# Performance work log

Hardware: AMD Instinct MI355X
Metric: run time of the kernel (lower is better)

The kernel has to match this reference:

```python
import jax, jax.numpy as jnp
import numpy as np

BIDAT = 4


def _biatt(atoms_vector, amino_vector, U, Wp2c, bp2c, Wc2p, bc2p,
           Whc, bhc, Whp, bhp, Wac, bac, Wap, bap, Wcc, bcc, Wcp, bcp):
    cfs, pfs = [], []
    for i in range(BIDAT):  # fixed small structural loop (4 distinct param sets)
        # bilinear tanh affinity: [Na, Np]
        A = jnp.tanh((atoms_vector @ U[i]) @ amino_vector.T)
        atoms_trans = A @ jnp.tanh(amino_vector @ Wp2c[i] + bp2c[i])      # [Na, D]
        amino_trans = A.T @ jnp.tanh(atoms_vector @ Wc2p[i] + bc2p[i])    # [Np, D]
        atoms_tmp = jnp.concatenate(
            [jnp.tanh(atoms_vector @ Whc[i] + bhc[i]), atoms_trans], axis=1)  # [Na, 2D]
        amino_tmp = jnp.concatenate(
            [jnp.tanh(amino_vector @ Whp[i] + bhp[i]), amino_trans], axis=1)  # [Np, 2D]
        # NOTE: softmax over axis=1 of a [N,1] tensor == all-ones (faithful to torch source)
        atoms_att = jax.nn.softmax(atoms_tmp @ Wac[i] + bac[i], axis=1)   # [Na, 1]
        amino_att = jax.nn.softmax(amino_tmp @ Wap[i] + bap[i], axis=1)   # [Np, 1]
        cfs.append(atoms_vector * atoms_att)
        pfs.append(amino_vector * amino_att)
    cf_final = jnp.concatenate(cfs, axis=1) @ Wcc + bcc   # [Na, D]
    pf_final = jnp.concatenate(pfs, axis=1) @ Wcp + bcp   # [Np, D]
    return cf_final, pf_final


def setup_inputs() -> dict:
    D, Na, Np = 512, 6144, 6144
    key = jax.random.key(0)
    ks = jax.random.split(key, 20)
    s = 0.04  # ~xavier-scale init for D=512
    return {
        "atoms_vector": jax.random.normal(ks[0], (Na, D), jnp.float32),
        "amino_vector": jax.random.normal(ks[1], (Np, D), jnp.float32),
        "U":    jax.random.normal(ks[2], (BIDAT, D, D), jnp.float32) * s,
        "Wp2c": jax.random.normal(ks[3], (BIDAT, D, D), jnp.float32) * s,
        "bp2c": jnp.zeros((BIDAT, D), jnp.float32),
        "Wc2p": jax.random.normal(ks[4], (BIDAT, D, D), jnp.float32) * s,
        "bc2p": jnp.zeros((BIDAT, D), jnp.float32),
        "Whc":  jax.random.normal(ks[5], (BIDAT, D, D), jnp.float32) * s,
        "bhc":  jnp.zeros((BIDAT, D), jnp.float32),
        "Whp":  jax.random.normal(ks[6], (BIDAT, D, D), jnp.float32) * s,
        "bhp":  jnp.zeros((BIDAT, D), jnp.float32),
        "Wac":  jax.random.normal(ks[7], (BIDAT, 2 * D, 1), jnp.float32) * s,
        "bac":  jnp.zeros((BIDAT, 1), jnp.float32),
        "Wap":  jax.random.normal(ks[8], (BIDAT, 2 * D, 1), jnp.float32) * s,
        "bap":  jnp.zeros((BIDAT, 1), jnp.float32),
        "Wcc":  jax.random.normal(ks[9], (BIDAT * D, D), jnp.float32) * s,
        "bcc":  jnp.zeros((D,), jnp.float32),
        "Wcp":  jax.random.normal(ks[10], (BIDAT * D, D), jnp.float32) * s,
        "bcp":  jnp.zeros((D,), jnp.float32),
    }


def reference(atoms_vector, amino_vector, U, Wp2c, bp2c, Wc2p, bc2p,
              Whc, bhc, Whp, bhp, Wac, bac, Wap, bap, Wcc, bcc, Wcp, bcp):
    return _biatt(atoms_vector, amino_vector, U, Wp2c, bp2c, Wc2p, bc2p,
                  Whc, bhc, Whp, bhp, Wac, bac, Wap, bap, Wcc, bcc, Wcp, bcp)
```

## Files before the change

kernel.cpp:

```cpp
#include <hip/hip_runtime.h>
#include <hip/hip_bf16.h>

#define DDIM 512
#define NROWS 6144
#define BM 64
#define BN 128
#define BK 32
#define KSTEPS (DDIM / BK)

typedef __attribute__((ext_vector_type(8))) short short8;
typedef __attribute__((ext_vector_type(4))) float f32x4;

#define GLDS16(g, s)                                          \
  __builtin_amdgcn_global_load_lds(                           \
      (const __attribute__((address_space(1))) void*)(g),     \
      (__attribute__((address_space(3))) void*)(s), 16, 0, 0)

__global__ __launch_bounds__(256) void prep_w(
    const float* __restrict__ Wcc, const float* __restrict__ Wcp,
    __hip_bfloat16* __restrict__ Wt) {
    const float* W = blockIdx.z ? Wcp : Wcc;
    unsigned short* o = (unsigned short*)Wt + (size_t)blockIdx.z * DDIM * DDIM;
    __shared__ float lds[32][65];
    const int k0 = blockIdx.x * 32, n0 = blockIdx.y * 64;
    #pragma unroll
    for (int u = 0; u < 2; ++u) {
        int idx = u * 256 + threadIdx.x;
        int kk = idx >> 4, c = idx & 15;
        float4 s = {0.f, 0.f, 0.f, 0.f};
        #pragma unroll
        for (int i = 0; i < 4; ++i) {
            float4 v = *(const float4*)&W[(size_t)(i * DDIM + k0 + kk) * DDIM + n0 + c * 4];
            s.x += v.x; s.y += v.y; s.z += v.z; s.w += v.w;
        }
        lds[kk][c * 4 + 0] = s.x;
        lds[kk][c * 4 + 1] = s.y;
        lds[kk][c * 4 + 2] = s.z;
        lds[kk][c * 4 + 3] = s.w;
    }
    __syncthreads();
    #pragma unroll
    for (int u = 0; u < 2; ++u) {
        int idx = u * 256 + threadIdx.x;
        int nr = idx >> 3, kc = idx & 7;
        ushort4 p;
        #pragma unroll
        for (int j = 0; j < 4; ++j) {
            __hip_bfloat16 h = __float2bfloat16(lds[kc * 4 + j][nr]);
            ((unsigned short*)&p)[j] = *(unsigned short*)&h;
        }
        *(ushort4*)&o[(size_t)(n0 + nr) * DDIM + k0 + kc * 4] = p;
    }
}

__global__ __launch_bounds__(256, 3) void gemm_bias(
    const float* __restrict__ Aat, const float* __restrict__ Aam,
    const __hip_bfloat16* __restrict__ Wtall,
    const float* __restrict__ bias0, const float* __restrict__ bias1,
    float* __restrict__ C) {
  __shared__ float As[3][BM * BK];
  __shared__ unsigned short Bs[3][BN * BK];

  const int z = blockIdx.z;
  const float* A = z ? Aam : Aat;
  const unsigned short* Wt = (const unsigned short*)Wtall + (size_t)z * DDIM * DDIM;
  const float* bias = z ? bias1 : bias0;
  float* Cz = C + (size_t)z * NROWS * DDIM;

  const int tid = threadIdx.x;
  const int w = tid >> 6, l = tid & 63;
  const int m0 = blockIdx.x * BM;
  const int n0 = blockIdx.y * BN;

  const float* srcA0;
  const float* srcA1;
  const unsigned short* srcB0;
  const unsigned short* srcB1;
  {
    int r0 = w * 16 + (l >> 3);
    int r1 = r0 + 8;
    srcA0 = A + (size_t)(m0 + r0) * DDIM + (((l & 7) ^ (r0 & 7)) << 2);
    srcA1 = A + (size_t)(m0 + r1) * DDIM + (((l & 7) ^ (r1 & 7)) << 2);
    int q0 = w * 32 + (l >> 2);
    int q1 = q0 + 16;
    srcB0 = Wt + (size_t)(n0 + q0) * DDIM + (((l & 3) ^ ((q0 >> 1) & 3)) << 3);
    srcB1 = Wt + (size_t)(n0 + q1) * DDIM + (((l & 3) ^ ((q1 >> 1) & 3)) << 3);
  }
  const unsigned ldsA0 = (w * 2 + 0) * 256, ldsA1 = (w * 2 + 1) * 256;
  const unsigned ldsB0 = (w * 2 + 0) * 512, ldsB1 = (w * 2 + 1) * 512;

#define STAGE(buf, kk)                                 \
  do {                                                 \
    GLDS16(srcA0 + (kk) * BK, &As[buf][ldsA0]);        \
    GLDS16(srcA1 + (kk) * BK, &As[buf][ldsA1]);        \
    GLDS16(srcB0 + (kk) * BK, &Bs[buf][ldsB0]);        \
    GLDS16(srcB1 + (kk) * BK, &Bs[buf][ldsB1]);        \
  } while (0)

  f32x4 acc[2][4];
  #pragma unroll
  for (int i = 0; i < 2; ++i)
    #pragma unroll
    for (int j = 0; j < 4; ++j) acc[i][j] = (f32x4){0.f, 0.f, 0.f, 0.f};

  const int s0 = (l >> 4) * 2;
  const int bs = (l >> 4);
  const int lr = l & 15;

#define COMPUTE(buf)                                                          \
  do {                                                                        \
    short8 afr[2];                                                            \
    _Pragma("unroll")                                                         \
    for (int tm = 0; tm < 2; ++tm) {                                          \
      int r = (w >> 1) * 32 + tm * 16 + lr;                                   \
      f32x4 x0 = *(const f32x4*)&As[buf][r * BK + (((s0 + 0) ^ (r & 7)) << 2)]; \
      f32x4 x1 = *(const f32x4*)&As[buf][r * BK + (((s0 + 1) ^ (r & 7)) << 2)]; \
      float xv[8] = {x0[0], x0[1], x0[2], x0[3], x1[0], x1[1], x1[2], x1[3]}; \
      _Pragma("unroll")                                                       \
      for (int e = 0; e < 8; ++e) {                                           \
        __hip_bfloat16 h = __float2bfloat16(xv[e]);                           \
        afr[tm][e] = *(short*)&h;                                             \
      }                                                                       \
    }                                                                         \
    _Pragma("unroll")                                                         \
    for (int tn = 0; tn < 4; ++tn) {                                          \
      int r = (w & 1) * 64 + tn * 16 + lr;                                    \
      short8 bf = *(const short8*)&Bs[buf][r * BK + ((bs ^ ((r >> 1) & 3)) << 3)]; \
      acc[0][tn] = __builtin_amdgcn_mfma_f32_16x16x32_bf16(afr[0], bf, acc[0][tn], 0, 0, 0); \
      acc[1][tn] = __builtin_amdgcn_mfma_f32_16x16x32_bf16(afr[1], bf, acc[1][tn], 0, 0, 0); \
    }                                                                         \
  } while (0)

  STAGE(0, 0);
  STAGE(1, 1);

  #pragma unroll
  for (int t = 0; t < KSTEPS; ++t) {
    if (t < KSTEPS - 1)
      asm volatile("s_waitcnt vmcnt(4)" ::: "memory");
    else
      asm volatile("s_waitcnt vmcnt(0)" ::: "memory");
    __builtin_amdgcn_s_barrier();
    if (t + 2 < KSTEPS) STAGE((t + 2) % 3, t + 2);
    COMPUTE(t % 3);
  }

  const int rg = (l >> 4) * 4;
  #pragma unroll
  for (int tn = 0; tn < 4; ++tn) {
    const int col = n0 + (w & 1) * 64 + tn * 16 + lr;
    const float bv = bias[col];
    #pragma unroll
    for (int tm = 0; tm < 2; ++tm) {
      const int row = m0 + (w >> 1) * 32 + tm * 16 + rg;
      #pragma unroll
      for (int r = 0; r < 4; ++r)
        Cz[(size_t)(row + r) * DDIM + col] = acc[tm][tn][r] + bv;
    }
  }
#undef STAGE
#undef COMPUTE
}

extern "C" void kernel_launch(void* const* d_in, const int* in_sizes, int n_in,
                              void* d_out, int out_size, void* d_ws, size_t ws_size,
                              hipStream_t stream) {
    const float* atoms = (const float*)d_in[0];
    const float* amino = (const float*)d_in[1];
    const float* Wcc   = (const float*)d_in[15];
    const float* bcc   = (const float*)d_in[16];
    const float* Wcp   = (const float*)d_in[17];
    const float* bcp   = (const float*)d_in[18];
    float* out = (float*)d_out;

    __hip_bfloat16* Wt = (__hip_bfloat16*)d_ws;

    dim3 fgrid(DDIM / 32, DDIM / 64, 2);
    prep_w<<<fgrid, 256, 0, stream>>>(Wcc, Wcp, Wt);

    dim3 ggrid(NROWS / BM, DDIM / BN, 2);
    gemm_bias<<<ggrid, 256, 0, stream>>>(atoms, amino, Wt, bcc, bcp, out);
}
```

Baseline: 134.1 us.

## Keep full weight panel resident in LDS and drop per-step block barriers

The GEMM tile shrinks to 64x64. The block's entire 64x512 bf16 weight panel is now loaded into LDS once up front, replacing the per-k-step staging of B tiles. Each wave streams and converts only its own 16 activation rows through a private double buffer. That removes the block-wide barrier from the k-loop, leaving only vmcnt/lgkmcnt waits. In exchange, the grid doubles, each activation row is read twice as many times from L2/HBM, per-wave MFMA work per step drops, and LDS use rises to roughly 80KB per block, which limits occupancy to two blocks.

```diff
diff --git a/kernel.cpp b/kernel.cpp
--- a/kernel.cpp
+++ b/kernel.cpp
@@ -4,7 +4,7 @@
 #define DDIM 512
 #define NROWS 6144
 #define BM 64
-#define BN 128
+#define BN 64
 #define BK 32
 #define KSTEPS (DDIM / BK)
 
@@ -53,13 +53,13 @@
     }
 }
 
-__global__ __launch_bounds__(256, 3) void gemm_bias(
+__global__ __launch_bounds__(256, 2) void gemm_bias(
     const float* __restrict__ Aat, const float* __restrict__ Aam,
     const __hip_bfloat16* __restrict__ Wtall,
     const float* __restrict__ bias0, const float* __restrict__ bias1,
     float* __restrict__ C) {
-  __shared__ float As[3][BM * BK];
-  __shared__ unsigned short Bs[3][BN * BK];
+  __shared__ unsigned short Bs[BN * DDIM];
+  __shared__ float As[2][BM * BK];
 
   const int z = blockIdx.z;
   const float* A = z ? Aam : Aat;
@@ -69,97 +69,81 @@
 
   const int tid = threadIdx.x;
   const int w = tid >> 6, l = tid & 63;
-  const int m0 = blockIdx.x * BM;
-  const int n0 = blockIdx.y * BN;
+  const int lr = l & 15, hi = l >> 4;
+  const int m0 = blockIdx.x * BM, n0 = blockIdx.y * BN;
 
-  const float* srcA0;
-  const float* srcA1;
-  const unsigned short* srcB0;
-  const unsigned short* srcB1;
-  {
-    int r0 = w * 16 + (l >> 3);
-    int r1 = r0 + 8;
-    srcA0 = A + (size_t)(m0 + r0) * DDIM + (((l & 7) ^ (r0 & 7)) << 2);
-    srcA1 = A + (size_t)(m0 + r1) * DDIM + (((l & 7) ^ (r1 & 7)) << 2);
-    int q0 = w * 32 + (l >> 2);
-    int q1 = q0 + 16;
-    srcB0 = Wt + (size_t)(n0 + q0) * DDIM + (((l & 3) ^ ((q0 >> 1) & 3)) << 3);
-    srcB1 = Wt + (size_t)(n0 + q1) * DDIM + (((l & 3) ^ ((q1 >> 1) & 3)) << 3);
+  #pragma unroll
+  for (int r = 0; r < 16; ++r) {
+    const int row = w * 16 + r;
+    GLDS16(Wt + (size_t)(n0 + row) * DDIM + ((l ^ (row & 7)) << 3),
+           &Bs[row * DDIM]);
   }
-  const unsigned ldsA0 = (w * 2 + 0) * 256, ldsA1 = (w * 2 + 1) * 256;
-  const unsigned ldsB0 = (w * 2 + 0) * 512, ldsB1 = (w * 2 + 1) * 512;
 
-#define STAGE(buf, kk)                                 \
-  do {                                                 \
-    GLDS16(srcA0 + (kk) * BK, &As[buf][ldsA0]);        \
-    GLDS16(srcA1 + (kk) * BK, &As[buf][ldsA1]);        \
-    GLDS16(srcB0 + (kk) * BK, &Bs[buf][ldsB0]);        \
-    GLDS16(srcB1 + (kk) * BK, &Bs[buf][ldsB1]);        \
-  } while (0)
+  const int ra0 = w * 16 + (l >> 3), ra1 = ra0 + 8;
+  const float* srcA0 = A + (size_t)(m0 + ra0) * DDIM + (((l & 7) ^ (ra0 & 7)) << 2);
+  const float* srcA1 = A + (size_t)(m0 + ra1) * DDIM + (((l & 7) ^ (ra1 & 7)) << 2);
+  const unsigned ldsA0 = (w * 16) * BK, ldsA1 = (w * 16 + 8) * BK;
 
-  f32x4 acc[2][4];
-  #pragma unroll
-  for (int i = 0; i < 2; ++i)
-    #pragma unroll
-    for (int j = 0; j < 4; ++j) acc[i][j] = (f32x4){0.f, 0.f, 0.f, 0.f};
-
-  const int s0 = (l >> 4) * 2;
-  const int bs = (l >> 4);
-  const int lr = l & 15;
-
-#define COMPUTE(buf)                                                          \
-  do {                                                                        \
-    short8 afr[2];                                                            \
-    _Pragma("unroll")                                                         \
-    for (int tm = 0; tm < 2; ++tm) {                                          \
-      int r = (w >> 1) * 32 + tm * 16 + lr;                                   \
-      f32x4 x0 = *(const f32x4*)&As[buf][r * BK + (((s0 + 0) ^ (r & 7)) << 2)]; \
-      f32x4 x1 = *(const f32x4*)&As[buf][r * BK + (((s0 + 1) ^ (r & 7)) << 2)]; \
-      float xv[8] = {x0[0], x0[1], x0[2], x0[3], x1[0], x1[1], x1[2], x1[3]}; \
-      _Pragma("unroll")                                                       \
-      for (int e = 0; e < 8; ++e) {                                           \
-        __hip_bfloat16 h = __float2bfloat16(xv[e]);                           \
-        afr[tm][e] = *(short*)&h;                                             \
-      }                                                                       \
-    }                                                                         \
-    _Pragma("unroll")                                                         \
-    for (int tn = 0; tn < 4; ++tn) {                                          \
-      int r = (w & 1) * 64 + tn * 16 + lr;                                    \
-      short8 bf = *(const short8*)&Bs[buf][r * BK + ((bs ^ ((r >> 1) & 3)) << 3)]; \
-      acc[0][tn] = __builtin_amdgcn_mfma_f32_16x16x32_bf16(afr[0], bf, acc[0][tn], 0, 0, 0); \
-      acc[1][tn] = __builtin_amdgcn_mfma_f32_16x16x32_bf16(afr[1], bf, acc[1][tn], 0, 0, 0); \
-    }                                                                         \
+#define STAGE(buf, kk)                              \
+  do {                                              \
+    GLDS16(srcA0 + (kk) * BK, &As[buf][ldsA0]);     \
+    GLDS16(srcA1 + (kk) * BK, &As[buf][ldsA1]);     \
   } while (0)
 
   STAGE(0, 0);
   STAGE(1, 1);
 
+  f32x4 acc[4];
+  #pragma unroll
+  for (int j = 0; j < 4; ++j) acc[j] = (f32x4){0.f, 0.f, 0.f, 0.f};
+
+  asm volatile("s_waitcnt vmcnt(4)" ::: "memory");
+  __builtin_amdgcn_s_barrier();
+
   #pragma unroll
   for (int t = 0; t < KSTEPS; ++t) {
     if (t < KSTEPS - 1)
-      asm volatile("s_waitcnt vmcnt(4)" ::: "memory");
+      asm volatile("s_waitcnt vmcnt(2)" ::: "memory");
     else
       asm volatile("s_waitcnt vmcnt(0)" ::: "memory");
-    __builtin_amdgcn_s_barrier();
-    if (t + 2 < KSTEPS) STAGE((t + 2) % 3, t + 2);
-    COMPUTE(t % 3);
+    const int buf = t & 1;
+
+    const int r = w * 16 + lr;
+    f32x4 x0 = *(const f32x4*)&As[buf][r * BK + (((hi * 2 + 0) ^ (lr & 7)) << 2)];
+    f32x4 x1 = *(const f32x4*)&As[buf][r * BK + (((hi * 2 + 1) ^ (lr & 7)) << 2)];
+    short8 af;
+    {
+      float xv[8] = {x0[0], x0[1], x0[2], x0[3], x1[0], x1[1], x1[2], x1[3]};
+      #pragma unroll
+      for (int e = 0; e < 8; ++e) {
+        __hip_bfloat16 h = __float2bfloat16(xv[e]);
+        af[e] = *(short*)&h;
+      }
+    }
+    #pragma unroll
+    for (int tn = 0; tn < 4; ++tn) {
+      const int np = tn * 16 + lr;
+      const int slot = (t * 4 + hi) ^ (lr & 7);
+      short8 bf = *(const short8*)&Bs[np * DDIM + slot * 8];
+      acc[tn] = __builtin_amdgcn_mfma_f32_16x16x32_bf16(af, bf, acc[tn], 0, 0, 0);
+    }
+
+    if (t + 2 < KSTEPS) {
+      asm volatile("s_waitcnt lgkmcnt(0)" ::: "memory");
+      __builtin_amdgcn_sched_barrier(0);
+      STAGE(buf, t + 2);
+    }
   }
 
-  const int rg = (l >> 4) * 4;
   #pragma unroll
   for (int tn = 0; tn < 4; ++tn) {
-    const int col = n0 + (w & 1) * 64 + tn * 16 + lr;
+    const int col = n0 + tn * 16 + lr;
     const float bv = bias[col];
     #pragma unroll
-    for (int tm = 0; tm < 2; ++tm) {
-      const int row = m0 + (w >> 1) * 32 + tm * 16 + rg;
-      #pragma unroll
-      for (int r = 0; r < 4; ++r)
-        Cz[(size_t)(row + r) * DDIM + col] = acc[tm][tn][r] + bv;
-    }
+    for (int rr = 0; rr < 4; ++rr)
+      Cz[(size_t)(m0 + w * 16 + hi * 4 + rr) * DDIM + col] = acc[tn][rr] + bv;
   }
 #undef STAGE
-#undef COMPUTE
 }
 
 extern "C" void kernel_launch(void* const* d_in, const int* in_sizes, int n_in,
```

Result: slower. 147.2 us (+9.7%).
